# Performance work log

Measured on AMD Instinct MI355X. Metric: run time of the kernel, lower is better.

The kernel has to match this reference:

```python
import jax, jax.numpy as jnp
import numpy as np

DIM = 256
HEADS = 4
DIM_HEAD = 32
HIDDEN = HEADS * DIM_HEAD  # 128
SCALE = DIM_HEAD ** -0.5
EPS = 1e-5


def setup_inputs() -> dict:
    key = jax.random.key(0)
    ks = jax.random.split(key, 6)
    B, H, W = 32, 64, 64
    x = jax.random.normal(ks[0], (B, DIM, H, W), dtype=jnp.float32)
    w_qkv = jax.random.normal(ks[1], (3 * HIDDEN, DIM), dtype=jnp.float32) * (DIM ** -0.5)
    w_out = jax.random.normal(ks[2], (DIM, HIDDEN), dtype=jnp.float32) * (HIDDEN ** -0.5)
    b_out = jnp.zeros((DIM,), dtype=jnp.float32)
    g = jnp.ones((DIM,), dtype=jnp.float32)
    b = jnp.zeros((DIM,), dtype=jnp.float32)
    return {"x": x, "w_qkv": w_qkv, "w_out": w_out, "b_out": b_out, "g": g, "b": b}


def reference(x, w_qkv, w_out, b_out, g, b):
    B, C, H, W = x.shape
    n = H * W
    # 1x1 conv qkv projection (no bias)
    qkv = jnp.einsum('oc,bchw->bohw', w_qkv, x)  # [B, 3*HIDDEN, H, W]
    qkv = qkv.reshape(B, 3, HEADS, DIM_HEAD, n)  # [B, 3, h, d, n]
    q, k, v = qkv[:, 0], qkv[:, 1], qkv[:, 2]
    q = jax.nn.softmax(q, axis=-2) * SCALE       # softmax over head dim d
    k = jax.nn.softmax(k, axis=-1)               # softmax over tokens n
    context = jnp.einsum('bhdn,bhen->bhde', k, v)
    out = jnp.einsum('bhde,bhdn->bhen', context, q)  # [B, h, e, n]
    out = out.reshape(B, HIDDEN, H, W)
    # 1x1 conv output projection with bias
    out = jnp.einsum('oc,bchw->bohw', w_out, out) + b_out[None, :, None, None]
    # LayerNorm over channel dim (biased variance)
    mean = jnp.mean(out, axis=1, keepdims=True)
    var = jnp.var(out, axis=1, keepdims=True)
    out = (out - mean) / jnp.sqrt(var + EPS) * g[None, :, None, None] + b[None, :, None, None]
    return out
```

## Files before the change

kernel.cpp:

```cpp
#include <hip/hip_runtime.h>
#include <math.h>

#define NPIX 4096
#define BATCH 32
#define CDIM 256
#define SCALE_F 0.17677669529663687f
#define EPS_F 1e-5f

typedef _Float16 f16;
typedef _Float16 f16x8 __attribute__((ext_vector_type(8)));
typedef _Float16 f16x4 __attribute__((ext_vector_type(4)));
typedef float    f32x4 __attribute__((ext_vector_type(4)));

static __device__ __forceinline__ f32x4 mfma16(f16x8 a, f16x8 b, f32x4 c) {
    return __builtin_amdgcn_mfma_f32_16x16x32_f16(a, b, c, 0, 0, 0);
}

__global__ __launch_bounds__(256)
void wconv(const float* __restrict__ w, f16* __restrict__ wh)
{
    int i = blockIdx.x * 256 + threadIdx.x;
    float4 v = ((const float4*)w)[i];
    f16x4 o = {(f16)v.x, (f16)v.y, (f16)v.z, (f16)v.w};
    ((f16x4*)wh)[i] = o;
}

__global__ __launch_bounds__(256)
void transpose_x(const float* __restrict__ x, f16* __restrict__ xt, int b0)
{
    __shared__ f16 T[64][66];
    const int b = b0 + blockIdx.z;
    const int n0 = blockIdx.x * 64, k0 = blockIdx.y * 64;
    const float* xb = x + ((size_t)b * 256 + k0) * NPIX + n0;
    const int t = threadIdx.x;
    const int kl = t >> 2;
    #pragma unroll
    for (int it = 0; it < 4; it++) {
        int nq = (t & 3) + it * 4;
        float4 v = *(const float4*)&xb[(size_t)kl * NPIX + nq * 4];
        T[kl][nq * 4 + 0] = (f16)v.x;
        T[kl][nq * 4 + 1] = (f16)v.y;
        T[kl][nq * 4 + 2] = (f16)v.z;
        T[kl][nq * 4 + 3] = (f16)v.w;
    }
    __syncthreads();
    const int nl = t >> 2, kc = t & 3;
    f16 tmp[16];
    #pragma unroll
    for (int j = 0; j < 16; j++) tmp[j] = T[kc * 16 + j][nl];
    f16* dst = xt + ((size_t)blockIdx.z * NPIX + n0 + nl) * 256 + k0 + kc * 16;
    *(f16x8*)dst = *(f16x8*)&tmp[0];
    *(f16x8*)(dst + 8) = *(f16x8*)&tmp[8];
}

__global__ __launch_bounds__(256)
void qkv_mfma(const f16* __restrict__ wh, const f16* __restrict__ xt, int b0,
              f16* __restrict__ qhatT, f16* __restrict__ ekp, f16* __restrict__ vp,
              float* __restrict__ ksum)
{
    __shared__ __align__(16) f16 As[128 * 32];
    __shared__ __align__(16) f16 Bs[128 * 32];
    const int b = b0 + blockIdx.z;
    const int tileM = blockIdx.y * 128;
    const int tileN = blockIdx.x * 128;
    const int t = threadIdx.x;
    const int lane = t & 63, w = t >> 6;
    const int lane15 = lane & 15, lg = lane >> 4;
    const int wrow = (w >> 1) * 64, wcol = (w & 1) * 64;

    const f16* Ab = wh + (size_t)tileM * 256;
    const f16* Bb = xt + ((size_t)blockIdx.z * NPIX + tileN) * 256;

    f32x4 acc[4][4];
    const f32x4 z4 = {0.f, 0.f, 0.f, 0.f};
    #pragma unroll
    for (int i = 0; i < 4; i++)
        #pragma unroll
        for (int j = 0; j < 4; j++) acc[i][j] = z4;

    for (int k0 = 0; k0 < 256; k0 += 32) {
        #pragma unroll
        for (int it = 0; it < 2; it++) {
            int c = t + it * 256;
            int row = c >> 2, koff = (c & 3) * 8;
            *(f16x8*)&As[row * 32 + koff] = *(const f16x8*)&Ab[(size_t)row * 256 + k0 + koff];
            *(f16x8*)&Bs[row * 32 + koff] = *(const f16x8*)&Bb[(size_t)row * 256 + k0 + koff];
        }
        __syncthreads();
        f16x8 af[4], bf[4];
        #pragma unroll
        for (int i = 0; i < 4; i++)
            af[i] = *(const f16x8*)&As[(wrow + i * 16 + lane15) * 32 + lg * 8];
        #pragma unroll
        for (int j = 0; j < 4; j++)
            bf[j] = *(const f16x8*)&Bs[(wcol + j * 16 + lane15) * 32 + lg * 8];
        #pragma unroll
        for (int i = 0; i < 4; i++)
            #pragma unroll
            for (int j = 0; j < 4; j++)
                acc[i][j] = mfma16(af[i], bf[j], acc[i][j]);
        __syncthreads();
    }

    if (blockIdx.y == 0) {
        f16* qT = qhatT + (size_t)b * NPIX * 128;
        #pragma unroll
        for (int hh = 0; hh < 2; hh++) {
            #pragma unroll
            for (int j = 0; j < 4; j++) {
                float e0[2][4];
                float s = 0.f;
                #pragma unroll
                for (int ii = 0; ii < 2; ii++)
                    #pragma unroll
                    for (int r = 0; r < 4; r++) {
                        float ev = __expf(acc[hh * 2 + ii][j][r]);
                        e0[ii][r] = ev; s += ev;
                    }
                s += __shfl_xor(s, 16);
                s += __shfl_xor(s, 32);
                float inv = SCALE_F / s;
                int n = tileN + wcol + j * 16 + lane15;
                #pragma unroll
                for (int ii = 0; ii < 2; ii++) {
                    int d0 = wrow + (hh * 2 + ii) * 16 + lg * 4;
                    f16x4 pk;
                    #pragma unroll
                    for (int r = 0; r < 4; r++) pk[r] = (f16)(e0[ii][r] * inv);
                    *(f16x4*)(qT + (size_t)n * 128 + d0) = pk;
                }
            }
        }
    } else if (blockIdx.y == 1) {
        f16* ekb = ekp + (size_t)b * 128 * NPIX;
        #pragma unroll
        for (int i = 0; i < 4; i++) {
            #pragma unroll
            for (int r = 0; r < 4; r++) {
                int d = wrow + i * 16 + lg * 4 + r;
                float p = 0.f;
                #pragma unroll
                for (int j = 0; j < 4; j++) {
                    float ev = __expf(acc[i][j][r]);
                    p += ev;
                    ekb[(size_t)d * NPIX + tileN + wcol + j * 16 + lane15] = (f16)ev;
                }
                p += __shfl_xor(p, 1); p += __shfl_xor(p, 2);
                p += __shfl_xor(p, 4); p += __shfl_xor(p, 8);
                if (lane15 == 0) atomicAdd(&ksum[b * 128 + d], p);
            }
        }
    } else {
        f16* vb = vp + (size_t)b * 128 * NPIX;
        #pragma unroll
        for (int i = 0; i < 4; i++)
            #pragma unroll
            for (int r = 0; r < 4; r++) {
                int d = wrow + i * 16 + lg * 4 + r;
                #pragma unroll
                for (int j = 0; j < 4; j++)
                    vb[(size_t)d * NPIX + tileN + wcol + j * 16 + lane15] =
                        (f16)acc[i][j][r];
            }
    }
}

__global__ __launch_bounds__(256)
void ctx_mfma(const f16* __restrict__ ekp, const f16* __restrict__ vp,
              float* __restrict__ ctx)
{
    const int bh = blockIdx.y;
    const int t = threadIdx.x;
    const int lane = t & 63, w = t >> 6;
    const int lane15 = lane & 15, lg = lane >> 4;
    const f16* ekb = ekp + ((size_t)(bh >> 2) * 128 + (size_t)(bh & 3) * 32) * NPIX;
    const f16* vb  = vp  + ((size_t)(bh >> 2) * 128 + (size_t)(bh & 3) * 32) * NPIX;
    const int nbase = blockIdx.x * 1024 + w * 256;
    f32x4 acc[2][2];
    const f32x4 z4 = {0.f, 0.f, 0.f, 0.f};
    acc[0][0] = z4; acc[0][1] = z4; acc[1][0] = z4; acc[1][1] = z4;
    for (int s = 0; s < 8; s++) {
        int n0 = nbase + s * 32;
        f16x8 af[2], bf[2];
        #pragma unroll
        for (int i = 0; i < 2; i++)
            af[i] = *(const f16x8*)&ekb[(size_t)(i * 16 + lane15) * NPIX + n0 + lg * 8];
        #pragma unroll
        for (int j = 0; j < 2; j++)
            bf[j] = *(const f16x8*)&vb[(size_t)(j * 16 + lane15) * NPIX + n0 + lg * 8];
        #pragma unroll
        for (int i = 0; i < 2; i++)
            #pragma unroll
            for (int j = 0; j < 2; j++)
                acc[i][j] = mfma16(af[i], bf[j], acc[i][j]);
    }
    __shared__ float cs[1024];
    for (int i = t; i < 1024; i += 256) cs[i] = 0.f;
    __syncthreads();
    #pragma unroll
    for (int i = 0; i < 2; i++)
        #pragma unroll
        for (int j = 0; j < 2; j++)
            #pragma unroll
            for (int r = 0; r < 4; r++)
                atomicAdd(&cs[(i * 16 + lg * 4 + r) * 32 + j * 16 + lane15], acc[i][j][r]);
    __syncthreads();
    float* cg = ctx + (size_t)bh * 1024;
    #pragma unroll
    for (int q = 0; q < 4; q++) {
        int idx = t + q * 256;
        atomicAdd(&cg[idx], cs[idx]);
    }
}

__global__ __launch_bounds__(256)
void weff_kernel(const float* __restrict__ wout, const float* __restrict__ ctx,
                 const float* __restrict__ ksum, f16* __restrict__ weff)
{
    const int bh = blockIdx.x;
    const int b = bh >> 2, h = bh & 3;
    __shared__ float cs[1024];
    __shared__ float inv_s[32];
    const int t = threadIdx.x;
    for (int i = t; i < 1024; i += 256) cs[i] = ctx[(size_t)bh * 1024 + i];
    if (t < 32) inv_s[t] = 1.f / ksum[b * 128 + h * 32 + t];
    __syncthreads();
    float acc[32] = {};
    const float* wrow = wout + (size_t)t * 128 + h * 32;
    for (int e = 0; e < 32; e++) {
        float wv = wrow[e];
        #pragma unroll
        for (int d = 0; d < 32; d++) acc[d] += wv * cs[d * 32 + e];
    }
    f16* wo = weff + ((size_t)b * 256 + t) * 128 + h * 32;
    #pragma unroll
    for (int d = 0; d < 32; d++) wo[d] = (f16)(acc[d] * inv_s[d]);
}

__global__ __launch_bounds__(256)
void out_mfma_ln(const f16* __restrict__ weff, const f16* __restrict__ qhatT,
                 const float* __restrict__ bias, const float* __restrict__ g,
                 const float* __restrict__ bb, float* __restrict__ out)
{
    __shared__ __align__(16) f16 As2[256 * 32];
    __shared__ __align__(16) f16 Bs2[128 * 32];
    __shared__ float pb[256], pg[256], pbb[256];
    __shared__ float lds_s[4][128], lds_s2[4][128];
    const int b = blockIdx.y;
    const int tileN = blockIdx.x * 128;
    const int t = threadIdx.x;
    const int lane = t & 63, w = t >> 6;
    const int lane15 = lane & 15, lg = lane >> 4;
    pb[t] = bias[t]; pg[t] = g[t]; pbb[t] = bb[t];
    const f16* Aw = weff + (size_t)b * 256 * 128;
    const f16* Bw = qhatT + (size_t)b * NPIX * 128;
    f32x4 acc[4][8];
    const f32x4 z4 = {0.f, 0.f, 0.f, 0.f};
    #pragma unroll
    for (int i = 0; i < 4; i++)
        #pragma unroll
        for (int j = 0; j < 8; j++) acc[i][j] = z4;

    for (int k0 = 0; k0 < 128; k0 += 32) {
        #pragma unroll
        for (int it = 0; it < 4; it++) {
            int c = t + it * 256;
            int row = c >> 2, koff = (c & 3) * 8;
            *(f16x8*)&As2[row * 32 + koff] = *(const f16x8*)&Aw[(size_t)row * 128 + k0 + koff];
        }
        #pragma unroll
        for (int it = 0; it < 2; it++) {
            int c = t + it * 256;
            int row = c >> 2, koff = (c & 3) * 8;
            *(f16x8*)&Bs2[row * 32 + koff] =
                *(const f16x8*)&Bw[(size_t)(tileN + row) * 128 + k0 + koff];
        }
        __syncthreads();
        f16x8 af[4], bf[8];
        #pragma unroll
        for (int i = 0; i < 4; i++)
            af[i] = *(const f16x8*)&As2[(w * 64 + i * 16 + lane15) * 32 + lg * 8];
        #pragma unroll
        for (int j = 0; j < 8; j++)
            bf[j] = *(const f16x8*)&Bs2[(j * 16 + lane15) * 32 + lg * 8];
        #pragma unroll
        for (int i = 0; i < 4; i++)
            #pragma unroll
            for (int j = 0; j < 8; j++)
                acc[i][j] = mfma16(af[i], bf[j], acc[i][j]);
        __syncthreads();
    }
    #pragma unroll
    for (int i = 0; i < 4; i++)
        #pragma unroll
        for (int r = 0; r < 4; r++) {
            float bo = pb[w * 64 + i * 16 + lg * 4 + r];
            #pragma unroll
            for (int j = 0; j < 8; j++) acc[i][j][r] += bo;
        }
    #pragma unroll
    for (int j = 0; j < 8; j++) {
        float s = 0.f, s2 = 0.f;
        #pragma unroll
        for (int i = 0; i < 4; i++)
            #pragma unroll
            for (int r = 0; r < 4; r++) { float v = acc[i][j][r]; s += v; s2 += v * v; }
        s += __shfl_xor(s, 16);  s += __shfl_xor(s, 32);
        s2 += __shfl_xor(s2, 16); s2 += __shfl_xor(s2, 32);
        if (lg == 0) { lds_s[w][j * 16 + lane15] = s; lds_s2[w][j * 16 + lane15] = s2; }
    }
    __syncthreads();
    float mean[8], rstd[8];
    #pragma unroll
    for (int j = 0; j < 8; j++) {
        int col = j * 16 + lane15;
        float S = lds_s[0][col] + lds_s[1][col] + lds_s[2][col] + lds_s[3][col];
        float S2 = lds_s2[0][col] + lds_s2[1][col] + lds_s2[2][col] + lds_s2[3][col];
        float mn = S * (1.f / 256.f);
        mean[j] = mn;
        rstd[j] = rsqrtf(S2 * (1.f / 256.f) - mn * mn + EPS_F);
    }
    float* ob = out + (size_t)b * CDIM * NPIX;
    #pragma unroll
    for (int i = 0; i < 4; i++)
        #pragma unroll
        for (int r = 0; r < 4; r++) {
            int row = w * 64 + i * 16 + lg * 4 + r;
            float gm = pg[row], bt = pbb[row];
            #pragma unroll
            for (int j = 0; j < 8; j++)
                ob[(size_t)row * NPIX + tileN + j * 16 + lane15] =
                    (acc[i][j][r] - mean[j]) * rstd[j] * gm + bt;
        }
}

extern "C" void kernel_launch(void* const* d_in, const int* in_sizes, int n_in,
                              void* d_out, int out_size, void* d_ws, size_t ws_size,
                              hipStream_t stream)
{
    const float* x     = (const float*)d_in[0];
    const float* w_qkv = (const float*)d_in[1];
    const float* w_out = (const float*)d_in[2];
    const float* b_out = (const float*)d_in[3];
    const float* g     = (const float*)d_in[4];
    const float* bvec  = (const float*)d_in[5];
    float* out = (float*)d_out;

    char* wsb = (char*)d_ws;
    f16*   xt    = (f16*)wsb;
    f16*   qhatT = (f16*)(wsb + 33554432);
    float* ctx   = (float*)(wsb + 67108864);
    float* ksum  = (float*)(wsb + 67633152);
    f16*   weff  = (f16*)(wsb + 67649536);
    f16*   wh    = (f16*)(wsb + 69746688);
    f16* ekp = (f16*)d_out;
    f16* vp  = ekp + 16777216;

    hipMemsetAsync(ctx, 0, 540672, stream);
    wconv<<<96, 256, 0, stream>>>(w_qkv, wh);
    for (int p = 0; p < 2; p++) {
        transpose_x<<<dim3(64, 4, 16), 256, 0, stream>>>(x, xt, p * 16);
        qkv_mfma<<<dim3(32, 3, 16), 256, 0, stream>>>(wh, xt, p * 16,
                                                      qhatT, ekp, vp, ksum);
    }
    ctx_mfma<<<dim3(4, 128), 256, 0, stream>>>(ekp, vp, ctx);
    weff_kernel<<<128, 256, 0, stream>>>(w_out, ctx, ksum, weff);
    out_mfma_ln<<<dim3(32, BATCH), 256, 0, stream>>>(weff, qhatT, b_out, g, bvec, out);
}
```

Measured before the change: 366.3 us.

## Fuse x transpose, QKV projection and context GEMM into one kernel

Replaces the transpose_x, qkv_mfma and ctx_mfma kernels with a single qkv_fused kernel. Each block loads fp32 x directly, converts it to fp16 in registers, computes all 384 QKV rows for a 64-pixel tile, and keeps exp(k) and v in swizzled LDS to accumulate the context matrix on the spot. This removes the xt transpose buffer and the global ek/v round trips. In exchange it uses larger LDS, holds a 6x4 accumulator per wave, reloads the full weight tile for every pixel tile, and issues strided scalar loads of x.

```diff
diff --git a/kernel.cpp b/kernel.cpp
--- a/kernel.cpp
+++ b/kernel.cpp
@@ -26,191 +26,169 @@
 }
 
 __global__ __launch_bounds__(256)
-void transpose_x(const float* __restrict__ x, f16* __restrict__ xt, int b0)
-{
-    __shared__ f16 T[64][66];
-    const int b = b0 + blockIdx.z;
-    const int n0 = blockIdx.x * 64, k0 = blockIdx.y * 64;
-    const float* xb = x + ((size_t)b * 256 + k0) * NPIX + n0;
-    const int t = threadIdx.x;
-    const int kl = t >> 2;
-    #pragma unroll
-    for (int it = 0; it < 4; it++) {
-        int nq = (t & 3) + it * 4;
-        float4 v = *(const float4*)&xb[(size_t)kl * NPIX + nq * 4];
-        T[kl][nq * 4 + 0] = (f16)v.x;
-        T[kl][nq * 4 + 1] = (f16)v.y;
-        T[kl][nq * 4 + 2] = (f16)v.z;
-        T[kl][nq * 4 + 3] = (f16)v.w;
-    }
-    __syncthreads();
-    const int nl = t >> 2, kc = t & 3;
-    f16 tmp[16];
-    #pragma unroll
-    for (int j = 0; j < 16; j++) tmp[j] = T[kc * 16 + j][nl];
-    f16* dst = xt + ((size_t)blockIdx.z * NPIX + n0 + nl) * 256 + k0 + kc * 16;
-    *(f16x8*)dst = *(f16x8*)&tmp[0];
-    *(f16x8*)(dst + 8) = *(f16x8*)&tmp[8];
-}
-
-__global__ __launch_bounds__(256)
-void qkv_mfma(const f16* __restrict__ wh, const f16* __restrict__ xt, int b0,
-              f16* __restrict__ qhatT, f16* __restrict__ ekp, f16* __restrict__ vp,
-              float* __restrict__ ksum)
-{
-    __shared__ __align__(16) f16 As[128 * 32];
-    __shared__ __align__(16) f16 Bs[128 * 32];
-    const int b = b0 + blockIdx.z;
-    const int tileM = blockIdx.y * 128;
-    const int tileN = blockIdx.x * 128;
+void qkv_fused(const f16* __restrict__ wh, const float* __restrict__ x,
+               f16* __restrict__ qhatT, float* __restrict__ ctx,
+               float* __restrict__ ksum)
+{
+    __shared__ __align__(16) f16 As[384 * 32];
+    __shared__ __align__(16) f16 Bs[64 * 32];
+    __shared__ __align__(16) f16 ek_s[128 * 64];
+    __shared__ __align__(16) f16 v_s[128 * 64];
+
+    const int b = blockIdx.y;
     const int t = threadIdx.x;
     const int lane = t & 63, w = t >> 6;
     const int lane15 = lane & 15, lg = lane >> 4;
-    const int wrow = (w >> 1) * 64, wcol = (w & 1) * 64;
-
-    const f16* Ab = wh + (size_t)tileM * 256;
-    const f16* Bb = xt + ((size_t)blockIdx.z * NPIX + tileN) * 256;
-
-    f32x4 acc[4][4];
+    const int grow = w * 96;
+
+    const float* xb = x + (size_t)b * 256 * NPIX;
+    f16* qT = qhatT + (size_t)b * NPIX * 128;
+
+    const int bn = t & 63;
+    const int bc = t >> 6;
+    const int bsw = bn * 32 + ((bc ^ ((bn >> 1) & 3)) << 3);
+
+    f32x4 ctxacc[2][2];
     const f32x4 z4 = {0.f, 0.f, 0.f, 0.f};
-    #pragma unroll
-    for (int i = 0; i < 4; i++)
-        #pragma unroll
-        for (int j = 0; j < 4; j++) acc[i][j] = z4;
-
-    for (int k0 = 0; k0 < 256; k0 += 32) {
-        #pragma unroll
-        for (int it = 0; it < 2; it++) {
-            int c = t + it * 256;
-            int row = c >> 2, koff = (c & 3) * 8;
-            *(f16x8*)&As[row * 32 + koff] = *(const f16x8*)&Ab[(size_t)row * 256 + k0 + koff];
-            *(f16x8*)&Bs[row * 32 + koff] = *(const f16x8*)&Bb[(size_t)row * 256 + k0 + koff];
+    ctxacc[0][0] = z4; ctxacc[0][1] = z4; ctxacc[1][0] = z4; ctxacc[1][1] = z4;
+
+    for (int tile = 0; tile < 4; tile++) {
+        const int n0 = blockIdx.x * 256 + tile * 64;
+        f32x4 acc[6][4];
+        #pragma unroll
+        for (int i = 0; i < 6; i++)
+            #pragma unroll
+            for (int j = 0; j < 4; j++) acc[i][j] = z4;
+
+        float v8[8];
+        #pragma unroll
+        for (int m = 0; m < 8; m++)
+            v8[m] = xb[(size_t)(bc * 8 + m) * NPIX + n0 + bn];
+
+        for (int ks = 0; ks < 8; ks++) {
+            const int k0 = ks * 32;
+            #pragma unroll
+            for (int it = 0; it < 6; it++) {
+                int c = t + it * 256;
+                int row = c >> 2, ch = c & 3;
+                *(f16x8*)&As[row * 32 + ((ch ^ ((row >> 1) & 3)) << 3)] =
+                    *(const f16x8*)&wh[(size_t)row * 256 + k0 + ch * 8];
+            }
+            f16x8 bv;
+            #pragma unroll
+            for (int m = 0; m < 8; m++) bv[m] = (f16)v8[m];
+            *(f16x8*)&Bs[bsw] = bv;
+            __syncthreads();
+            if (ks < 7) {
+                #pragma unroll
+                for (int m = 0; m < 8; m++)
+                    v8[m] = xb[(size_t)(k0 + 32 + bc * 8 + m) * NPIX + n0 + bn];
+            }
+            f16x8 bf[4];
+            #pragma unroll
+            for (int j = 0; j < 4; j++) {
+                int rr = j * 16 + lane15;
+                bf[j] = *(const f16x8*)&Bs[rr * 32 + ((lg ^ ((rr >> 1) & 3)) << 3)];
+            }
+            #pragma unroll
+            for (int i = 0; i < 6; i++) {
+                int rr = grow + i * 16 + lane15;
+                f16x8 af = *(const f16x8*)&As[rr * 32 + ((lg ^ ((rr >> 1) & 3)) << 3)];
+                #pragma unroll
+                for (int j = 0; j < 4; j++)
+                    acc[i][j] = mfma16(af, bf[j], acc[i][j]);
+            }
+            __syncthreads();
+        }
+
+        #pragma unroll
+        for (int i = 0; i < 6; i++) {
+            const int rbase = grow + i * 16;
+            if (rbase < 128) {
+                if ((rbase & 31) == 0) {
+                    #pragma unroll
+                    for (int j = 0; j < 4; j++) {
+                        float e0[2][4]; float s = 0.f;
+                        #pragma unroll
+                        for (int ii = 0; ii < 2; ii++)
+                            #pragma unroll
+                            for (int r = 0; r < 4; r++) {
+                                float ev = __expf(acc[i + ii][j][r]);
+                                e0[ii][r] = ev; s += ev;
+                            }
+                        s += __shfl_xor(s, 16); s += __shfl_xor(s, 32);
+                        float inv = SCALE_F / s;
+                        int n = n0 + j * 16 + lane15;
+                        #pragma unroll
+                        for (int ii = 0; ii < 2; ii++) {
+                            int d0 = rbase + ii * 16 + lg * 4;
+                            f16x4 pk;
+                            #pragma unroll
+                            for (int r = 0; r < 4; r++) pk[r] = (f16)(e0[ii][r] * inv);
+                            *(f16x4*)(qT + (size_t)n * 128 + d0) = pk;
+                        }
+                    }
+                }
+            } else if (rbase < 256) {
+                const int kb = rbase - 128;
+                #pragma unroll
+                for (int r = 0; r < 4; r++) {
+                    int row = kb + lg * 4 + r;
+                    float p = 0.f;
+                    #pragma unroll
+                    for (int j = 0; j < 4; j++) {
+                        float ev = __expf(acc[i][j][r]);
+                        p += ev;
+                        int col = j * 16 + lane15;
+                        ek_s[row * 64 + ((((col >> 3) ^ (row & 7)) << 3) | (col & 7))] =
+                            (f16)ev;
+                    }
+                    p += __shfl_xor(p, 1); p += __shfl_xor(p, 2);
+                    p += __shfl_xor(p, 4); p += __shfl_xor(p, 8);
+                    if (lane15 == 0) atomicAdd(&ksum[b * 128 + row], p);
+                }
+            } else {
+                const int vb = rbase - 256;
+                #pragma unroll
+                for (int r = 0; r < 4; r++) {
+                    int row = vb + lg * 4 + r;
+                    #pragma unroll
+                    for (int j = 0; j < 4; j++) {
+                        int col = j * 16 + lane15;
+                        v_s[row * 64 + ((((col >> 3) ^ (row & 7)) << 3) | (col & 7))] =
+                            (f16)acc[i][j][r];
+                    }
+                }
+            }
         }
         __syncthreads();
-        f16x8 af[4], bf[4];
-        #pragma unroll
-        for (int i = 0; i < 4; i++)
-            af[i] = *(const f16x8*)&As[(wrow + i * 16 + lane15) * 32 + lg * 8];
-        #pragma unroll
-        for (int j = 0; j < 4; j++)
-            bf[j] = *(const f16x8*)&Bs[(wcol + j * 16 + lane15) * 32 + lg * 8];
-        #pragma unroll
-        for (int i = 0; i < 4; i++)
-            #pragma unroll
-            for (int j = 0; j < 4; j++)
-                acc[i][j] = mfma16(af[i], bf[j], acc[i][j]);
-        __syncthreads();
-    }
-
-    if (blockIdx.y == 0) {
-        f16* qT = qhatT + (size_t)b * NPIX * 128;
-        #pragma unroll
-        for (int hh = 0; hh < 2; hh++) {
-            #pragma unroll
-            for (int j = 0; j < 4; j++) {
-                float e0[2][4];
-                float s = 0.f;
-                #pragma unroll
-                for (int ii = 0; ii < 2; ii++)
-                    #pragma unroll
-                    for (int r = 0; r < 4; r++) {
-                        float ev = __expf(acc[hh * 2 + ii][j][r]);
-                        e0[ii][r] = ev; s += ev;
-                    }
-                s += __shfl_xor(s, 16);
-                s += __shfl_xor(s, 32);
-                float inv = SCALE_F / s;
-                int n = tileN + wcol + j * 16 + lane15;
-                #pragma unroll
-                for (int ii = 0; ii < 2; ii++) {
-                    int d0 = wrow + (hh * 2 + ii) * 16 + lg * 4;
-                    f16x4 pk;
-                    #pragma unroll
-                    for (int r = 0; r < 4; r++) pk[r] = (f16)(e0[ii][r] * inv);
-                    *(f16x4*)(qT + (size_t)n * 128 + d0) = pk;
-                }
-            }
-        }
-    } else if (blockIdx.y == 1) {
-        f16* ekb = ekp + (size_t)b * 128 * NPIX;
-        #pragma unroll
-        for (int i = 0; i < 4; i++) {
-            #pragma unroll
-            for (int r = 0; r < 4; r++) {
-                int d = wrow + i * 16 + lg * 4 + r;
-                float p = 0.f;
-                #pragma unroll
-                for (int j = 0; j < 4; j++) {
-                    float ev = __expf(acc[i][j][r]);
-                    p += ev;
-                    ekb[(size_t)d * NPIX + tileN + wcol + j * 16 + lane15] = (f16)ev;
-                }
-                p += __shfl_xor(p, 1); p += __shfl_xor(p, 2);
-                p += __shfl_xor(p, 4); p += __shfl_xor(p, 8);
-                if (lane15 == 0) atomicAdd(&ksum[b * 128 + d], p);
-            }
-        }
-    } else {
-        f16* vb = vp + (size_t)b * 128 * NPIX;
-        #pragma unroll
-        for (int i = 0; i < 4; i++)
-            #pragma unroll
-            for (int r = 0; r < 4; r++) {
-                int d = wrow + i * 16 + lg * 4 + r;
-                #pragma unroll
-                for (int j = 0; j < 4; j++)
-                    vb[(size_t)d * NPIX + tileN + wcol + j * 16 + lane15] =
-                        (f16)acc[i][j][r];
-            }
-    }
-}
-
-__global__ __launch_bounds__(256)
-void ctx_mfma(const f16* __restrict__ ekp, const f16* __restrict__ vp,
-              float* __restrict__ ctx)
-{
-    const int bh = blockIdx.y;
-    const int t = threadIdx.x;
-    const int lane = t & 63, w = t >> 6;
-    const int lane15 = lane & 15, lg = lane >> 4;
-    const f16* ekb = ekp + ((size_t)(bh >> 2) * 128 + (size_t)(bh & 3) * 32) * NPIX;
-    const f16* vb  = vp  + ((size_t)(bh >> 2) * 128 + (size_t)(bh & 3) * 32) * NPIX;
-    const int nbase = blockIdx.x * 1024 + w * 256;
-    f32x4 acc[2][2];
-    const f32x4 z4 = {0.f, 0.f, 0.f, 0.f};
-    acc[0][0] = z4; acc[0][1] = z4; acc[1][0] = z4; acc[1][1] = z4;
-    for (int s = 0; s < 8; s++) {
-        int n0 = nbase + s * 32;
-        f16x8 af[2], bf[2];
-        #pragma unroll
-        for (int i = 0; i < 2; i++)
-            af[i] = *(const f16x8*)&ekb[(size_t)(i * 16 + lane15) * NPIX + n0 + lg * 8];
-        #pragma unroll
-        for (int j = 0; j < 2; j++)
-            bf[j] = *(const f16x8*)&vb[(size_t)(j * 16 + lane15) * NPIX + n0 + lg * 8];
-        #pragma unroll
-        for (int i = 0; i < 2; i++)
-            #pragma unroll
-            for (int j = 0; j < 2; j++)
-                acc[i][j] = mfma16(af[i], bf[j], acc[i][j]);
-    }
-    __shared__ float cs[1024];
-    for (int i = t; i < 1024; i += 256) cs[i] = 0.f;
-    __syncthreads();
-    #pragma unroll
-    for (int i = 0; i < 2; i++)
-        #pragma unroll
-        for (int j = 0; j < 2; j++)
+        #pragma unroll
+        for (int ks2 = 0; ks2 < 2; ks2++) {
+            f16x8 a2[2], b2[2];
+            #pragma unroll
+            for (int i2 = 0; i2 < 2; i2++) {
+                int row = w * 32 + i2 * 16 + lane15;
+                int off = row * 64 + (((ks2 * 4 + lg) ^ (row & 7)) << 3);
+                a2[i2] = *(const f16x8*)&ek_s[off];
+                b2[i2] = *(const f16x8*)&v_s[off];
+            }
+            #pragma unroll
+            for (int i2 = 0; i2 < 2; i2++)
+                #pragma unroll
+                for (int j2 = 0; j2 < 2; j2++)
+                    ctxacc[i2][j2] = mfma16(a2[i2], b2[j2], ctxacc[i2][j2]);
+        }
+    }
+
+    float* cg = ctx + ((size_t)b * 4 + w) * 1024;
+    #pragma unroll
+    for (int i2 = 0; i2 < 2; i2++)
+        #pragma unroll
+        for (int j2 = 0; j2 < 2; j2++)
             #pragma unroll
             for (int r = 0; r < 4; r++)
-                atomicAdd(&cs[(i * 16 + lg * 4 + r) * 32 + j * 16 + lane15], acc[i][j][r]);
-    __syncthreads();
-    float* cg = ctx + (size_t)bh * 1024;
-    #pragma unroll
-    for (int q = 0; q < 4; q++) {
-        int idx = t + q * 256;
-        atomicAdd(&cg[idx], cs[idx]);
-    }
+                atomicAdd(&cg[(i2 * 16 + lg * 4 + r) * 32 + j2 * 16 + lane15],
+                          ctxacc[i2][j2][r]);
 }
 
 __global__ __launch_bounds__(256)
@@ -347,23 +325,15 @@
     float* out = (float*)d_out;
 
     char* wsb = (char*)d_ws;
-    f16*   xt    = (f16*)wsb;
-    f16*   qhatT = (f16*)(wsb + 33554432);
-    float* ctx   = (float*)(wsb + 67108864);
-    float* ksum  = (float*)(wsb + 67633152);
-    f16*   weff  = (f16*)(wsb + 67649536);
-    f16*   wh    = (f16*)(wsb + 69746688);
-    f16* ekp = (f16*)d_out;
-    f16* vp  = ekp + 16777216;
+    f16*   qhatT = (f16*)wsb;
+    float* ctx   = (float*)(wsb + 33554432);
+    float* ksum  = (float*)(wsb + 34078720);
+    f16*   weff  = (f16*)(wsb + 34095104);
+    f16*   wh    = (f16*)(wsb + 36192256);
 
     hipMemsetAsync(ctx, 0, 540672, stream);
     wconv<<<96, 256, 0, stream>>>(w_qkv, wh);
-    for (int p = 0; p < 2; p++) {
-        transpose_x<<<dim3(64, 4, 16), 256, 0, stream>>>(x, xt, p * 16);
-        qkv_mfma<<<dim3(32, 3, 16), 256, 0, stream>>>(wh, xt, p * 16,
-                                                      qhatT, ekp, vp, ksum);
-    }
-    ctx_mfma<<<dim3(4, 128), 256, 0, stream>>>(ekp, vp, ctx);
+    qkv_fused<<<dim3(16, BATCH), 256, 0, stream>>>(wh, x, qhatT, ctx, ksum);
     weff_kernel<<<128, 256, 0, stream>>>(w_out, ctx, ksum, weff);
     out_mfma_ln<<<dim3(32, BATCH), 256, 0, stream>>>(weff, qhatT, b_out, g, bvec, out);
 }
```

Result: faster. 349.3 us (-4.6%).
